# Kernel tuning notes

Hardware: AMD Instinct MI355X
Metric: run time of the kernel (lower is better)

Reference implementation:

```python
import jax, jax.numpy as jnp
import numpy as np

N_NODES = 50000
N_EDGES = 800000
IN_DIM = 256
HID = 256
NUM_LAYERS = 2


def _sage(xin, src, dst, inv_deg, W_l, b_l, W_r):
    # PyG SAGEConv (mean aggr): lin_l(mean of src features scattered to dst) + lin_r(x)
    agg = jax.ops.segment_sum(xin[src], dst, num_segments=xin.shape[0]) * inv_deg
    return agg @ W_l + b_l + xin @ W_r


def _mgdsgu(x, src, dst, inv_deg, h, Wx_l, bx_l, Wx_r, Wh_l, bh_l, Wh_r, Wb1, bb1, Wb2, bb2):
    # hid->hid conv order: 0=sage_hidden, 1=sage_single_h, 2=sage_update_h, 3=sage_candidate_h
    # in ->hid conv order: 0=sage_single_x, 1=sage_update_x, 2=sage_candidate_x
    h_N = _sage(h, src, dst, inv_deg, Wh_l[0], bh_l[0], Wh_r[0])
    # predict_missing_info: r = zeros so r_v = beta; gamma is computed in the
    # original but multiplied by zero -> no effect (omitted).
    beta = jnp.tanh(h @ Wb1 + bb1 + h_N @ Wb2 + bb2)
    m = h + beta - h_N
    h_N = h_N + m  # == h + beta, kept as written for clarity
    r = jax.nn.sigmoid(_sage(x, src, dst, inv_deg, Wx_l[0], bx_l[0], Wx_r[0])
                       + _sage(h_N, src, dst, inv_deg, Wh_l[1], bh_l[1], Wh_r[1]))
    z = jax.nn.sigmoid(_sage(x, src, dst, inv_deg, Wx_l[1], bx_l[1], Wx_r[1])
                       + _sage(h_N, src, dst, inv_deg, Wh_l[2], bh_l[2], Wh_r[2]))
    h_tilde = jnp.tanh(_sage(x, src, dst, inv_deg, Wx_l[2], bx_l[2], Wx_r[2])
                       + _sage(r * h_N, src, dst, inv_deg, Wh_l[3], bh_l[3], Wh_r[3]))
    return (1.0 - z) * h_N + z * h_tilde


def setup_inputs() -> dict:
    key = jax.random.key(0)
    ks = jax.random.split(key, 12)
    sx = 1.0 / np.sqrt(IN_DIM)
    sh = 1.0 / np.sqrt(HID)
    inp = {
        "x": jax.random.normal(ks[0], (N_NODES, IN_DIM), dtype=jnp.float32),
        "edge_index": jax.random.randint(ks[1], (2, N_EDGES), 0, N_NODES, dtype=jnp.int64),
        "Wx_l": jax.random.normal(ks[2], (3, IN_DIM, HID), dtype=jnp.float32) * sx,
        "bx_l": jnp.zeros((3, HID), dtype=jnp.float32),
        "Wx_r": jax.random.normal(ks[3], (3, IN_DIM, HID), dtype=jnp.float32) * sx,
        "Wh_l": jax.random.normal(ks[4], (4, HID, HID), dtype=jnp.float32) * sh,
        "bh_l": jnp.zeros((4, HID), dtype=jnp.float32),
        "Wh_r": jax.random.normal(ks[5], (4, HID, HID), dtype=jnp.float32) * sh,
        "Wb1": jax.random.normal(ks[6], (HID, HID), dtype=jnp.float32) * sh,
        "bb1": jnp.zeros((HID,), dtype=jnp.float32),
        "Wb2": jax.random.normal(ks[7], (HID, HID), dtype=jnp.float32) * sh,
        "bb2": jnp.zeros((HID,), dtype=jnp.float32),
        "We1": jax.random.normal(ks[8], (2 * HID, HID), dtype=jnp.float32) * (1.0 / np.sqrt(2 * HID)),
        "be1": jnp.zeros((HID,), dtype=jnp.float32),
        "We2": jax.random.normal(ks[9], (HID, 1), dtype=jnp.float32) * sh,
        "be2": jnp.zeros((1,), dtype=jnp.float32),
    }
    return inp


def reference(x, edge_index, Wx_l, bx_l, Wx_r, Wh_l, bh_l, Wh_r,
              Wb1, bb1, Wb2, bb2, We1, be1, We2, be2):
    src, dst = edge_index[0], edge_index[1]
    deg = jax.ops.segment_sum(jnp.ones((src.shape[0],), dtype=x.dtype), dst,
                              num_segments=x.shape[0])
    inv_deg = (1.0 / jnp.maximum(deg, 1.0))[:, None]  # [N, 1]

    h = jnp.zeros((x.shape[0], HID), dtype=x.dtype)
    for _ in range(NUM_LAYERS):
        h = _mgdsgu(x, src, dst, inv_deg, h, Wx_l, bx_l, Wx_r,
                    Wh_l, bh_l, Wh_r, Wb1, bb1, Wb2, bb2)

    # edge embeddings: concat(src emb, dst emb) -> MLP -> sigmoid
    edge_emb = jnp.concatenate([h[src], h[dst]], axis=1)  # [E, 2H]
    hidden = jax.nn.relu(edge_emb @ We1 + be1)
    preds = jax.nn.sigmoid(hidden @ We2 + be2)  # [E, 1]
    return (preds, h)
```

## Files before the change

### kernel.cpp

```cpp
#include <hip/hip_runtime.h>
#include <math.h>

#define HID 256
#define LROW 40

typedef __bf16 bf16x8 __attribute__((ext_vector_type(8)));
typedef float  f32x4  __attribute__((ext_vector_type(4)));
typedef unsigned short us8 __attribute__((ext_vector_type(8)));

__device__ __forceinline__ float sigmoidf_(float x){ return 1.0f/(1.0f + __expf(-x)); }
__device__ __forceinline__ unsigned short f2b(float f){
  __bf16 b = (__bf16)f; return __builtin_bit_cast(unsigned short, b);
}
__device__ __forceinline__ float b2f(unsigned short u){
  return (float)__builtin_bit_cast(__bf16, u);
}

__device__ __forceinline__ int edge_src(const int* ei, int e, int is64){
  return is64 ? ei[2*e] : ei[e];
}
__device__ __forceinline__ int edge_dst(const int* ei, int e, int E, int is64){
  return is64 ? ei[2*(E+e)] : ei[E+e];
}

__global__ void detect_kernel(const int* __restrict__ ei, int* __restrict__ flag){
  __shared__ int any;
  if (threadIdx.x == 0) any = 0;
  __syncthreads();
  if (ei[2*threadIdx.x + 1] != 0) atomicOr(&any, 1);
  __syncthreads();
  if (threadIdx.x == 0) *flag = any ? 0 : 1;
}

__global__ void count_kernel(const int* __restrict__ ei, const int* __restrict__ flag,
                             int* __restrict__ deg_i, int E){
  int e = blockIdx.x*blockDim.x + threadIdx.x;
  if (e >= E) return;
  int is64 = *flag;
  atomicAdd(&deg_i[edge_dst(ei,e,E,is64)], 1);
}

__global__ __launch_bounds__(1024) void scan_kernel(const int* __restrict__ deg_i,
  int* __restrict__ row_ptr, float* __restrict__ inv_deg, int N)
{
  __shared__ int wsum[16];
  __shared__ int carry_s;
  int tid = threadIdx.x, lane = tid & 63, wid = tid >> 6;
  if (tid == 0) carry_s = 0;
  __syncthreads();
  for (int base = 0; base < N; base += 1024){
    int i = base + tid;
    int v = (i < N) ? deg_i[i] : 0;
    int s = v;
    #pragma unroll
    for (int off = 1; off < 64; off <<= 1){
      int t = __shfl_up(s, off, 64);
      if (lane >= off) s += t;
    }
    if (lane == 63) wsum[wid] = s;
    __syncthreads();
    if (tid == 0){
      int run = 0;
      for (int w2 = 0; w2 < 16; ++w2){ int t = wsum[w2]; wsum[w2] = run; run += t; }
    }
    __syncthreads();
    int excl = carry_s + wsum[wid] + s - v;
    if (i < N){
      row_ptr[i] = excl;
      inv_deg[i] = 1.0f / fmaxf((float)v, 1.0f);
    }
    __syncthreads();
    if (tid == 1023) carry_s = excl + v;
    __syncthreads();
  }
  if (threadIdx.x == 0) row_ptr[N] = carry_s;
}

__global__ void fill_kernel(const int* __restrict__ ei, const int* __restrict__ flag,
                            const int* __restrict__ row_ptr, int* __restrict__ cursor,
                            int* __restrict__ col_src, int E){
  int e = blockIdx.x*blockDim.x + threadIdx.x;
  if (e >= E) return;
  int is64 = *flag;
  int d = edge_dst(ei,e,E,is64);
  int pos = atomicAdd(&cursor[d], 1);
  col_src[row_ptr[d] + pos] = edge_src(ei,e,is64);
}

__global__ __launch_bounds__(256) void conv_kernel(const float* __restrict__ in,
                                                   unsigned short* __restrict__ out, int n4){
  int i = blockIdx.x*256 + threadIdx.x;
  if (i >= n4) return;
  float4 v = *(const float4*)&in[(size_t)i*4];
  ushort4 o; o.x=f2b(v.x); o.y=f2b(v.y); o.z=f2b(v.z); o.w=f2b(v.w);
  *(ushort4*)&out[(size_t)i*4] = o;
}

__global__ __launch_bounds__(256) void wconv_kernel(
  const float* __restrict__ Wx_l, const float* __restrict__ Wx_r,
  const float* __restrict__ Wh_l, const float* __restrict__ Wh_r,
  const float* __restrict__ Wb1,  const float* __restrict__ Wb2,
  const float* __restrict__ We1,  unsigned short* __restrict__ Wt)
{
  int widx = blockIdx.x;
  int n = blockIdx.y;
  int k = threadIdx.x;
  const float* src;
  if      (widx < 3)  src = Wx_l + widx*65536;
  else if (widx < 6)  src = Wx_r + (widx-3)*65536;
  else if (widx < 10) src = Wh_l + (widx-6)*65536;
  else if (widx < 14) src = Wh_r + (widx-10)*65536;
  else if (widx == 14) src = Wb1;
  else if (widx == 15) src = Wb2;
  else                src = We1 + (widx-16)*65536;
  Wt[(size_t)widx*65536 + n*256 + k] = f2b(src[k*256 + n]);
}

__global__ __launch_bounds__(256) void comp_kernel(
  const float* __restrict__ A, const float* __restrict__ B,
  const float* __restrict__ add, unsigned short* __restrict__ dst)
{
  __shared__ float col[256];
  int n = blockIdx.x, k = threadIdx.x;
  col[k] = B[k*256 + n];
  __syncthreads();
  float s = add ? add[k*256 + n] : 0.f;
  #pragma unroll 8
  for (int j = 0; j < 256; ++j) s = fmaf(A[k*256 + j], col[j], s);
  dst[n*256 + k] = f2b(s);
}

__global__ __launch_bounds__(256) void aggregate_b_kernel(
    const unsigned short* __restrict__ X, unsigned short* __restrict__ out,
    const int* __restrict__ row_ptr, const int* __restrict__ col_src,
    const float* __restrict__ inv_deg, int N)
{
  int v = blockIdx.x*4 + (threadIdx.x >> 6);
  int lane = threadIdx.x & 63;
  if (v >= N) return;
  int beg = row_ptr[v], end = row_ptr[v+1];
  float a0=0.f, a1=0.f, a2=0.f, a3=0.f;
  int e = beg;
  for (; e + 8 <= end; e += 8){
    int sidx[8];
    #pragma unroll
    for (int t = 0; t < 8; ++t) sidx[t] = col_src[e + t];
    #pragma unroll
    for (int t = 0; t < 8; ++t){
      ushort4 u = *(const ushort4*)&X[(size_t)sidx[t]*HID + lane*4];
      a0 += b2f(u.x); a1 += b2f(u.y); a2 += b2f(u.z); a3 += b2f(u.w);
    }
  }
  for (; e < end; ++e){
    int s0 = col_src[e];
    ushort4 u = *(const ushort4*)&X[(size_t)s0*HID + lane*4];
    a0 += b2f(u.x); a1 += b2f(u.y); a2 += b2f(u.z); a3 += b2f(u.w);
  }
  float w = inv_deg[v];
  ushort4 o; o.x=f2b(a0*w); o.y=f2b(a1*w); o.z=f2b(a2*w); o.w=f2b(a3*w);
  *(ushort4*)&out[(size_t)v*HID + lane*4] = o;
}

__global__ __launch_bounds__(256) void rowprep_kernel(
  const float* __restrict__ bh_l, const float* __restrict__ bb1, const float* __restrict__ bb2,
  const float* __restrict__ Wb2, const float* __restrict__ Wh_l, const float* __restrict__ Wh_r,
  float* __restrict__ brow, float* __restrict__ hrow,
  float* __restrict__ rowL1, float* __restrict__ rowR1,
  float* __restrict__ rowL2, float* __restrict__ rowR2)
{
  __shared__ float sh[256];
  __shared__ float sh2[256];
  int j = threadIdx.x;
  sh[j] = bh_l[j];
  __syncthreads();
  float acc = bb1[j] + bb2[j];
  for (int k = 0; k < 256; ++k) acc = fmaf(sh[k], Wb2[k*256 + j], acc);
  float hr = tanhf(acc);
  brow[j] = acc;
  hrow[j] = hr; sh2[j] = hr;
  __syncthreads();
  const float* Whl1 = Wh_l + 65536;  const float* Whr1 = Wh_r + 65536;
  const float* Whl2 = Wh_l + 131072; const float* Whr2 = Wh_r + 131072;
  float a1=0.f, b1=0.f, a2=0.f, b2v=0.f;
  for (int k = 0; k < 256; ++k){
    float hv = sh2[k];
    a1  = fmaf(hv, Whl1[k*256+j], a1);
    b1  = fmaf(hv, Whr1[k*256+j], b1);
    a2  = fmaf(hv, Whl2[k*256+j], a2);
    b2v = fmaf(hv, Whr2[k*256+j], b2v);
  }
  rowL1[j] = a1; rowR1[j] = b1 + bh_l[256 + j];
  rowL2[j] = a2; rowR2[j] = b2v + bh_l[512 + j];
}

__global__ __launch_bounds__(256) void l1_elem_kernel(
  const unsigned short* __restrict__ xc0, const unsigned short* __restrict__ xc1,
  const int* __restrict__ deg_i, const float* __restrict__ hrow,
  const float* __restrict__ rowL1, const float* __restrict__ rowR1,
  const float* __restrict__ rowL2, const float* __restrict__ rowR2,
  unsigned short* __restrict__ t1, float* __restrict__ z1, int N)
{
  int idx = blockIdx.x*256 + threadIdx.x;
  if (idx >= N*64) return;
  int v = idx >> 6, j4 = (idx & 63) * 4;
  float g = deg_i[v] > 0 ? 1.f : 0.f;
  ushort4 a = *(const ushort4*)&xc0[(size_t)idx*4];
  ushort4 b = *(const ushort4*)&xc1[(size_t)idx*4];
  float4 L1 = *(const float4*)&rowL1[j4];
  float4 R1 = *(const float4*)&rowR1[j4];
  float4 L2 = *(const float4*)&rowL2[j4];
  float4 R2 = *(const float4*)&rowR2[j4];
  float4 hr = *(const float4*)&hrow[j4];
  ushort4 t; float4 z;
  t.x = f2b(sigmoidf_(b2f(a.x) + g*L1.x + R1.x) * hr.x);
  t.y = f2b(sigmoidf_(b2f(a.y) + g*L1.y + R1.y) * hr.y);
  t.z = f2b(sigmoidf_(b2f(a.z) + g*L1.z + R1.z) * hr.z);
  t.w = f2b(sigmoidf_(b2f(a.w) + g*L1.w + R1.w) * hr.w);
  z.x = sigmoidf_(b2f(b.x) + g*L2.x + R2.x);
  z.y = sigmoidf_(b2f(b.y) + g*L2.y + R2.y);
  z.z = sigmoidf_(b2f(b.z) + g*L2.z + R2.z);
  z.w = sigmoidf_(b2f(b.w) + g*L2.w + R2.w);
  *(ushort4*)&t1[(size_t)idx*4] = t;
  *(float4*)&z1[(size_t)idx*4] = z;
}

struct GJob {
  const unsigned short *A0,*W0,*A1,*W1;
  const float *bias,*Z,*HN;
  const float *mulmat;
  const unsigned short *Db,*Zb;
  float* outF; unsigned short* outB;
  int hn_bcast;
};

template<int MODE>
__global__ __launch_bounds__(512) void mgemm6_kernel(GJob j0, GJob j1, GJob j2, int M)
{
  __shared__ unsigned short Al[128*LROW];
  __shared__ unsigned short Wl[128*LROW];
  const int jidx = blockIdx.y >> 1;
  const GJob& J = (jidx == 0) ? j0 : ((jidx == 1) ? j1 : j2);
  const int col0 = (blockIdx.y & 1) * 128;
  const int tid  = threadIdx.x;
  const int lane = tid & 63, w = tid >> 6;
  const int wr = w >> 2, wc = w & 3;
  const int lane15 = lane & 15, laneq = (lane >> 4) * 8;
  const int row0 = blockIdx.x * 128;

  f32x4 acc[4][2];
  #pragma unroll
  for (int m = 0; m < 4; ++m)
    #pragma unroll
    for (int n = 0; n < 2; ++n) acc[m][n] = (f32x4)0.f;

  const unsigned short* pa[2]; const unsigned short* pw[2];
  int np = 0;
  if (J.A0){ pa[np]=J.A0; pw[np]=J.W0; ++np; }
  if (J.A1){ pa[np]=J.A1; pw[np]=J.W1; ++np; }
  const int steps = np * 8;

  const int strow = tid >> 2;
  const int koff  = (tid & 3) * 8;
  const int garow = (row0 + strow > M-1) ? (M-1) : (row0 + strow);
  const size_t abase = (size_t)garow*HID + koff;
  const size_t wbase = (size_t)(col0 + strow)*HID + koff;
  const int lidx = strow*LROW + koff;

  uint4 Ar0,Wr0, Ar1,Wr1;
  auto loadR = [&](int sp, uint4& a, uint4& wv){
    const unsigned short* Ap = pa[sp >> 3];
    const unsigned short* Wp = pw[sp >> 3];
    const int k0 = (sp & 7) * 32;
    a  = *(const uint4*)(Ap + abase + k0);
    wv = *(const uint4*)(Wp + wbase + k0);
  };
  auto compute = [&](){
    bf16x8 af[4], bfr[2];
    #pragma unroll
    for (int m = 0; m < 4; ++m)
      af[m] = *(const bf16x8*)&Al[(wr*64 + m*16 + lane15)*LROW + laneq];
    #pragma unroll
    for (int n = 0; n < 2; ++n)
      bfr[n] = *(const bf16x8*)&Wl[(wc*32 + n*16 + lane15)*LROW + laneq];
    #pragma unroll
    for (int m = 0; m < 4; ++m)
      #pragma unroll
      for (int n = 0; n < 2; ++n)
        acc[m][n] = __builtin_amdgcn_mfma_f32_16x16x32_bf16(af[m], bfr[n], acc[m][n], 0, 0, 0);
  };

  loadR(0, Ar0,Wr0);
  loadR(1, Ar1,Wr1);
  for (int s = 0; s < steps; s += 2){
    __syncthreads();
    *(uint4*)&Al[lidx] = Ar0;
    *(uint4*)&Wl[lidx] = Wr0;
    __syncthreads();
    if (s + 2 < steps) loadR(s+2, Ar0,Wr0);
    compute();
    __syncthreads();
    *(uint4*)&Al[lidx] = Ar1;
    *(uint4*)&Wl[lidx] = Wr1;
    __syncthreads();
    if (s + 3 < steps) loadR(s+3, Ar1,Wr1);
    compute();
  }

  #pragma unroll
  for (int n = 0; n < 2; ++n){
    int gc = col0 + wc*32 + n*16 + lane15;
    float badd = J.bias ? J.bias[gc] : 0.f;
    float hnb = 0.f;
    if (MODE == 3 && J.hn_bcast) hnb = J.HN[gc];
    #pragma unroll
    for (int m = 0; m < 4; ++m){
      int rbse = row0 + wr*64 + m*16 + ((lane >> 4) << 2);
      #pragma unroll
      for (int r = 0; r < 4; ++r){
        int gr = rbse + r;
        if (gr >= M) continue;
        size_t idx = (size_t)gr*HID + gc;
        float p = acc[m][n][r] + badd;
        if (J.Db) p += b2f(J.Db[idx]);
        float v;
        if (MODE == 0) v = p;
        else if (MODE == 1){
          v = sigmoidf_(p);
          if (J.mulmat) v *= J.mulmat[idx];
        } else if (MODE == 2){
          v = J.HN[idx] + tanhf(p);
        } else {
          float z  = J.Z ? J.Z[idx] : b2f(J.Zb[idx]);
          float hv = J.hn_bcast ? hnb : J.HN[idx];
          v = (1.f - z)*hv + z*tanhf(p);
        }
        if (J.outF) J.outF[idx] = v;
        if (J.outB) J.outB[idx] = f2b(v);
      }
    }
  }
}

__global__ __launch_bounds__(256) void edge_pred_kernel(
  const unsigned short* __restrict__ P, const unsigned short* __restrict__ Q,
  const int* __restrict__ ei, const int* __restrict__ flag,
  const float* __restrict__ We2, const float* __restrict__ be2,
  float* __restrict__ preds, int E)
{
  int wid = blockIdx.x*8 + (threadIdx.x >> 5);
  int l = threadIdx.x & 31;
  if (wid >= E) return;
  int is64 = *flag;
  int s = edge_src(ei, wid, is64);
  int d = edge_dst(ei, wid, E, is64);
  us8 p8 = *(const us8*)&P[(size_t)s*HID + l*8];
  us8 q8 = *(const us8*)&Q[(size_t)d*HID + l*8];
  float4 w0 = *(const float4*)&We2[l*8];
  float4 w1 = *(const float4*)&We2[l*8 + 4];
  float part = 0.f;
  #pragma unroll
  for (int j = 0; j < 4; ++j)
    part = fmaf(fmaxf(b2f(p8[j]) + b2f(q8[j]), 0.f), (&w0.x)[j], part);
  #pragma unroll
  for (int j = 0; j < 4; ++j)
    part = fmaf(fmaxf(b2f(p8[4+j]) + b2f(q8[4+j]), 0.f), (&w1.x)[j], part);
  #pragma unroll
  for (int off = 16; off > 0; off >>= 1) part += __shfl_down(part, off, 32);
  if (l == 0) preds[wid] = sigmoidf_(part + be2[0]);
}

typedef const unsigned short* cus;
typedef const float* cf;

template<int MODE>
static void launch_f(const GJob* j, int nj, int M, hipStream_t s){
  dim3 g((M + 127)/128, nj*2), blk(512);
  mgemm6_kernel<MODE><<<g, blk, 0, s>>>(j[0], nj > 1 ? j[1] : j[0], nj > 2 ? j[2] : j[0], M);
}

extern "C" void kernel_launch(void* const* d_in, const int* in_sizes, int n_in,
                              void* d_out, int out_size, void* d_ws, size_t ws_size,
                              hipStream_t stream)
{
  const float* x    = (const float*)d_in[0];
  const int*   ei   = (const int*)  d_in[1];
  const float* Wx_l = (const float*)d_in[2];
  const float* bx_l = (const float*)d_in[3];
  const float* Wx_r = (const float*)d_in[4];
  const float* Wh_l = (const float*)d_in[5];
  const float* bh_l = (const float*)d_in[6];
  const float* Wh_r = (const float*)d_in[7];
  const float* Wb1  = (const float*)d_in[8];
  const float* bb1  = (const float*)d_in[9];
  const float* Wb2  = (const float*)d_in[10];
  const float* bb2  = (const float*)d_in[11];
  const float* We1  = (const float*)d_in[12];
  const float* be1  = (const float*)d_in[13];
  const float* We2  = (const float*)d_in[14];
  const float* be2  = (const float*)d_in[15];

  const int N = in_sizes[0] / HID;
  const int E = in_sizes[1] / 2;
  cf NUL = nullptr; cus NUB = nullptr;

  size_t off = 0;
  auto alloc = [&](size_t bytes) -> void* {
    void* p = (char*)d_ws + off;
    off += (bytes + 255) & ~(size_t)255;
    return p;
  };
  int*   deg_i   = (int*)  alloc((size_t)N*4);
  int*   cursor  = (int*)  alloc((size_t)N*4);
  int*   row_ptr = (int*)  alloc(((size_t)N+1)*4);
  int*   col_src = (int*)  alloc((size_t)E*4);
  float* inv_deg = (float*)alloc((size_t)N*4);
  int*   flag    = (int*)  alloc(256);
  float* brow    = (float*)alloc(1024);
  float* hrow    = (float*)alloc(1024);
  float* rowL1   = (float*)alloc(1024);
  float* rowR1   = (float*)alloc(1024);
  float* rowL2   = (float*)alloc(1024);
  float* rowR2   = (float*)alloc(1024);
  unsigned short* Wt = (unsigned short*)alloc((size_t)18*65536*2);
  float* F1 = (float*)alloc((size_t)N*HID*4);
  unsigned short* b0 = (unsigned short*)alloc((size_t)N*HID*2);
  unsigned short* b1 = (unsigned short*)alloc((size_t)N*HID*2);
  unsigned short* b2 = (unsigned short*)alloc((size_t)N*HID*2);
  unsigned short* b3 = (unsigned short*)alloc((size_t)N*HID*2);
  unsigned short* b4 = (unsigned short*)alloc((size_t)N*HID*2);
  unsigned short* b5 = (unsigned short*)alloc((size_t)N*HID*2);

  float* preds = (float*)d_out;
  float* H     = preds + E;

  auto WT = [&](int i) -> cus { return Wt + (size_t)i*65536; };
  const float* bx0 = bx_l;  const float* bx1 = bx_l + 256; const float* bx2 = bx_l + 512;
  const float* bh1 = bh_l + 256;
  const float* bh2 = bh_l + 512; const float* bh3 = bh_l + 768;

  const int eb  = (E + 255)/256;
  const int nb4 = (N + 3)/4;
  const int n4b = (N*64 + 255)/256;

  auto mkjob = [&](cus A0,cus W0,cus A1,cus W1,
                   cf bias, cf Z, cf HN, int hnb,
                   cf mulmat, cus Db, cus Zb,
                   float* oF, unsigned short* oB) -> GJob {
    GJob g;
    g.A0=A0; g.W0=W0; g.A1=A1; g.W1=W1;
    g.bias=bias; g.Z=Z; g.HN=HN; g.hn_bcast=hnb;
    g.mulmat=mulmat; g.Db=Db; g.Zb=Zb;
    g.outF=oF; g.outB=oB;
    return g;
  };

  hipMemsetAsync(deg_i, 0, (size_t)N*4, stream);
  hipMemsetAsync(cursor, 0, (size_t)N*4, stream);
  detect_kernel<<<1,256,0,stream>>>(ei, flag);
  count_kernel<<<eb,256,0,stream>>>(ei, flag, deg_i, E);
  scan_kernel<<<1,1024,0,stream>>>(deg_i, row_ptr, inv_deg, N);
  fill_kernel<<<eb,256,0,stream>>>(ei, flag, row_ptr, cursor, col_src, E);

  conv_kernel<<<n4b,256,0,stream>>>(x, b0, N*64);
  wconv_kernel<<<dim3(18,256),256,0,stream>>>(Wx_l, Wx_r, Wh_l, Wh_r, Wb1, Wb2, We1, Wt);
  comp_kernel<<<256,256,0,stream>>>(Wh_l, Wb2, nullptr, (unsigned short*)WT(14));
  comp_kernel<<<256,256,0,stream>>>(Wh_r, Wb2, Wb1,     (unsigned short*)WT(15));
  rowprep_kernel<<<1,256,0,stream>>>(bh_l, bb1, bb2, Wb2, Wh_l, Wh_r,
                                     brow, hrow, rowL1, rowR1, rowL2, rowR2);

  aggregate_b_kernel<<<nb4,256,0,stream>>>(b0, b1, row_ptr, col_src, inv_deg, N);
  {
    GJob j[3] = {
      mkjob(b1,WT(0), b0,WT(3), bx0, NUL,NUL,0, NUL,NUB,NUB, nullptr, b2),
      mkjob(b1,WT(1), b0,WT(4), bx1, NUL,NUL,0, NUL,NUB,NUB, nullptr, b3),
      mkjob(b1,WT(2), b0,WT(5), bx2, NUL,NUL,0, NUL,NUB,NUB, nullptr, b4)
    };
    launch_f<0>(j, 3, N, stream);
  }

  l1_elem_kernel<<<n4b,256,0,stream>>>(b2, b3, deg_i, hrow, rowL1, rowR1,
                                       rowL2, rowR2, b0, F1, N);
  aggregate_b_kernel<<<nb4,256,0,stream>>>(b0, b1, row_ptr, col_src, inv_deg, N);
  {
    GJob j = mkjob(b1,WT(9), b0,WT(13), bh3, F1,hrow,1, NUL,b4,NUB, F1, b5);
    launch_f<3>(&j, 1, N, stream);
  }

  aggregate_b_kernel<<<nb4,256,0,stream>>>(b5, b0, row_ptr, col_src, inv_deg, N);
  {
    GJob j = mkjob(b0,WT(14), b5,WT(15), brow, NUL,F1,0, NUL,NUB,NUB, F1, b1);
    launch_f<2>(&j, 1, N, stream);
  }
  aggregate_b_kernel<<<nb4,256,0,stream>>>(b1, b0, row_ptr, col_src, inv_deg, N);
  {
    GJob j[2] = {
      mkjob(b0,WT(7), b1,WT(11), bh1, NUL,NUL,0, F1,b2,NUB, nullptr, b5),
      mkjob(b0,WT(8), b1,WT(12), bh2, NUL,NUL,0, NUL,b3,NUB, nullptr, b3)
    };
    launch_f<1>(j, 2, N, stream);
  }
  aggregate_b_kernel<<<nb4,256,0,stream>>>(b5, b0, row_ptr, col_src, inv_deg, N);
  {
    GJob j = mkjob(b0,WT(9), b5,WT(13), bh3, NUL,F1,0, NUL,b4,b3, H, b1);
    launch_f<3>(&j, 1, N, stream);
  }

  {
    GJob j[2] = {
      mkjob(b1,WT(16), NUB,NUB, be1, NUL,NUL,0, NUL,NUB,NUB, nullptr, b2),
      mkjob(b1,WT(17), NUB,NUB, NUL, NUL,NUL,0, NUL,NUB,NUB, nullptr, b5)
    };
    launch_f<0>(j, 2, N, stream);
  }
  edge_pred_kernel<<<(E+7)/8,256,0,stream>>>(b2, b5, ei, flag, We2, be2, preds, E);
}
```

Before: 1.147 ms.

## Remap GEMM blocks per XCD and process edge predictions in dst-sorted order

The GEMM grid is flattened into one dimension and remapped so that all column and job blocks sharing a row panel land on the same XCD (block id modulo 8). Sibling blocks can then reuse the A panel from that XCD's L2. The edge prediction kernel now walks edges in CSR (destination-sorted) order using new col_dst/col_eid arrays written by fill_kernel, so consecutive edges reuse the same Q row, and it scatters each result back to its original edge index. This costs two extra E-sized index arrays, the extra writes in fill_kernel, and scattered 4-byte prediction stores.

```diff
diff --git a/kernel.cpp b/kernel.cpp
--- a/kernel.cpp
+++ b/kernel.cpp
@@ -78,13 +78,17 @@
 
 __global__ void fill_kernel(const int* __restrict__ ei, const int* __restrict__ flag,
                             const int* __restrict__ row_ptr, int* __restrict__ cursor,
-                            int* __restrict__ col_src, int E){
+                            int* __restrict__ col_src, int* __restrict__ col_dst,
+                            int* __restrict__ col_eid, int E){
   int e = blockIdx.x*blockDim.x + threadIdx.x;
   if (e >= E) return;
   int is64 = *flag;
   int d = edge_dst(ei,e,E,is64);
   int pos = atomicAdd(&cursor[d], 1);
-  col_src[row_ptr[d] + pos] = edge_src(ei,e,is64);
+  int slot = row_ptr[d] + pos;
+  col_src[slot] = edge_src(ei,e,is64);
+  col_dst[slot] = d;
+  col_eid[slot] = e;
 }
 
 __global__ __launch_bounds__(256) void conv_kernel(const float* __restrict__ in,
@@ -234,18 +238,25 @@
 };
 
 template<int MODE>
-__global__ __launch_bounds__(512) void mgemm6_kernel(GJob j0, GJob j1, GJob j2, int M)
+__global__ __launch_bounds__(512) void mgemm6_kernel(GJob j0, GJob j1, GJob j2,
+                                                     int M, int NR, int NSIB)
 {
   __shared__ unsigned short Al[128*LROW];
   __shared__ unsigned short Wl[128*LROW];
-  const int jidx = blockIdx.y >> 1;
+  const int id   = blockIdx.x;
+  const int xcd  = id & 7;
+  const int sidx_= id >> 3;
+  const int jh   = sidx_ % NSIB;
+  const int rpan = (sidx_ / NSIB) * 8 + xcd;
+  if (rpan >= NR) return;
+  const int jidx = jh >> 1;
   const GJob& J = (jidx == 0) ? j0 : ((jidx == 1) ? j1 : j2);
-  const int col0 = (blockIdx.y & 1) * 128;
+  const int col0 = (jh & 1) * 128;
   const int tid  = threadIdx.x;
   const int lane = tid & 63, w = tid >> 6;
   const int wr = w >> 2, wc = w & 3;
   const int lane15 = lane & 15, laneq = (lane >> 4) * 8;
-  const int row0 = blockIdx.x * 128;
+  const int row0 = rpan * 128;
 
   f32x4 acc[4][2];
   #pragma unroll
@@ -343,16 +354,17 @@
 
 __global__ __launch_bounds__(256) void edge_pred_kernel(
   const unsigned short* __restrict__ P, const unsigned short* __restrict__ Q,
-  const int* __restrict__ ei, const int* __restrict__ flag,
+  const int* __restrict__ col_src, const int* __restrict__ col_dst,
+  const int* __restrict__ col_eid,
   const float* __restrict__ We2, const float* __restrict__ be2,
   float* __restrict__ preds, int E)
 {
-  int wid = blockIdx.x*8 + (threadIdx.x >> 5);
+  int slot = blockIdx.x*8 + (threadIdx.x >> 5);
   int l = threadIdx.x & 31;
-  if (wid >= E) return;
-  int is64 = *flag;
-  int s = edge_src(ei, wid, is64);
-  int d = edge_dst(ei, wid, E, is64);
+  if (slot >= E) return;
+  int s   = col_src[slot];
+  int d   = col_dst[slot];
+  int eid = col_eid[slot];
   us8 p8 = *(const us8*)&P[(size_t)s*HID + l*8];
   us8 q8 = *(const us8*)&Q[(size_t)d*HID + l*8];
   float4 w0 = *(const float4*)&We2[l*8];
@@ -366,7 +378,7 @@
     part = fmaf(fmaxf(b2f(p8[4+j]) + b2f(q8[4+j]), 0.f), (&w1.x)[j], part);
   #pragma unroll
   for (int off = 16; off > 0; off >>= 1) part += __shfl_down(part, off, 32);
-  if (l == 0) preds[wid] = sigmoidf_(part + be2[0]);
+  if (l == 0) preds[eid] = sigmoidf_(part + be2[0]);
 }
 
 typedef const unsigned short* cus;
@@ -374,8 +386,12 @@
 
 template<int MODE>
 static void launch_f(const GJob* j, int nj, int M, hipStream_t s){
-  dim3 g((M + 127)/128, nj*2), blk(512);
-  mgemm6_kernel<MODE><<<g, blk, 0, s>>>(j[0], nj > 1 ? j[1] : j[0], nj > 2 ? j[2] : j[0], M);
+  int NR = (M + 127)/128;
+  int RB = (NR + 7)/8;
+  int nsib = nj*2;
+  dim3 g(8*RB*nsib), blk(512);
+  mgemm6_kernel<MODE><<<g, blk, 0, s>>>(j[0], nj > 1 ? j[1] : j[0], nj > 2 ? j[2] : j[0],
+                                        M, NR, nsib);
 }
 
 extern "C" void kernel_launch(void* const* d_in, const int* in_sizes, int n_in,
@@ -413,6 +429,8 @@
   int*   cursor  = (int*)  alloc((size_t)N*4);
   int*   row_ptr = (int*)  alloc(((size_t)N+1)*4);
   int*   col_src = (int*)  alloc((size_t)E*4);
+  int*   col_dst = (int*)  alloc((size_t)E*4);
+  int*   col_eid = (int*)  alloc((size_t)E*4);
   float* inv_deg = (float*)alloc((size_t)N*4);
   int*   flag    = (int*)  alloc(256);
   float* brow    = (float*)alloc(1024);
@@ -459,7 +477,7 @@
   detect_kernel<<<1,256,0,stream>>>(ei, flag);
   count_kernel<<<eb,256,0,stream>>>(ei, flag, deg_i, E);
   scan_kernel<<<1,1024,0,stream>>>(deg_i, row_ptr, inv_deg, N);
-  fill_kernel<<<eb,256,0,stream>>>(ei, flag, row_ptr, cursor, col_src, E);
+  fill_kernel<<<eb,256,0,stream>>>(ei, flag, row_ptr, cursor, col_src, col_dst, col_eid, E);
 
   conv_kernel<<<n4b,256,0,stream>>>(x, b0, N*64);
   wconv_kernel<<<dim3(18,256),256,0,stream>>>(Wx_l, Wx_r, Wh_l, Wh_r, Wb1, Wb2, We1, Wt);
@@ -512,5 +530,6 @@
     };
     launch_f<0>(j, 2, N, stream);
   }
-  edge_pred_kernel<<<(E+7)/8,256,0,stream>>>(b2, b5, ei, flag, We2, be2, preds, E);
-}
+  edge_pred_kernel<<<(E+7)/8,256,0,stream>>>(b2, b5, col_src, col_dst, col_eid,
+                                             We2, be2, preds, E);
+}
```

New measurement: 1.233 ms. 1.08x slower.
